# Performance work log

Hardware: AMD Instinct MI355X
Metric: run time of the kernel (lower is better)

## Reference

```python
import jax, jax.numpy as jnp
import numpy as np

N = 8192
F_IN = 256
F_OUT = 64
ALPHA = 0.2  # LeakyReLU negative slope
EDGE_P = 0.004  # ~33 avg degree


def setup_inputs() -> dict:
    key = jax.random.key(0)
    k1, k2, k3, k4 = jax.random.split(key, 4)
    h = jax.random.normal(k1, (N, F_IN), dtype=jnp.float32)
    # xavier-ish scale for params
    W = jax.random.normal(k2, (F_IN, F_OUT), dtype=jnp.float32) * np.float32(np.sqrt(2.0 / (F_IN + F_OUT)))
    a = jax.random.normal(k3, (2 * F_OUT, 1), dtype=jnp.float32) * np.float32(np.sqrt(2.0 / (2 * F_OUT + 1)))
    adj = (jax.random.uniform(k4, (N, N)) < EDGE_P).astype(jnp.float32)
    return {"h": h, "adj": adj, "W": W, "a": a}


def reference(h, adj, W, a):
    f_out = W.shape[1]
    Wh = h @ W  # [N, F_OUT]
    # NOTE: original uses a[out_features:] for the source (row) term
    wh1 = Wh @ a[f_out:, :]  # [N, 1]
    wh2 = Wh @ a[:f_out, :]  # [N, 1]
    # e[u, i] = wh1[u] + wh2[i] only where adj nonzero; zero elsewhere (NO -inf mask,
    # faithful to the original: softmax sees zeros at non-edges)
    e = jnp.where(adj != 0, wh1 + wh2.T, jnp.float32(0.0))  # [N, N]
    e = jnp.where(e >= 0, e, ALPHA * e)  # LeakyReLU
    attention = jax.nn.softmax(e, axis=1)  # [N, N]
    # dropout p=0.0 -> identity
    h_prime = attention @ Wh  # [N, F_OUT]
    return jax.nn.elu(h_prime)  # concat=True
```

## Files before the change

### kernel.cpp

```cpp
#include <hip/hip_runtime.h>
#include <hip/hip_bf16.h>
#include <math.h>

#define N     8192
#define F_IN  256
#define F_OUT 64
#define ALPHA 0.2f

__global__ __launch_bounds__(256) void gat_wh_kernel(
    const float* __restrict__ h,
    const float* __restrict__ W,
    const float* __restrict__ a,
    float* __restrict__ Wh,
    float* __restrict__ wh1,
    float* __restrict__ wh2,
    float* __restrict__ colpart)
{
    __shared__ float s_h[4][F_IN];
    __shared__ float s_cp[256];

    const int tid = threadIdx.x;
    const int wv  = tid >> 6;
    const int ln  = tid & 63;
    const int u   = blockIdx.x * 4 + wv;

    const float4* hrow = (const float4*)(h + (size_t)u * F_IN);
    ((float4*)s_h[wv])[ln] = hrow[ln];
    __syncthreads();

    float acc = 0.f;
    const float4* sh4 = (const float4*)s_h[wv];
#pragma unroll 8
    for (int k4 = 0; k4 < F_IN / 4; ++k4) {
        float4 hv = sh4[k4];
        int k = k4 * 4;
        acc += hv.x * W[(k + 0) * F_OUT + ln];
        acc += hv.y * W[(k + 1) * F_OUT + ln];
        acc += hv.z * W[(k + 2) * F_OUT + ln];
        acc += hv.w * W[(k + 3) * F_OUT + ln];
    }

    Wh[(size_t)u * F_OUT + ln] = acc;

    float p1 = acc * a[F_OUT + ln];
    float p2 = acc * a[ln];
#pragma unroll
    for (int off = 32; off > 0; off >>= 1) {
        p1 += __shfl_down(p1, off);
        p2 += __shfl_down(p2, off);
    }
    if (ln == 0) {
        wh1[u] = p1;
        wh2[u] = p2;
    }

    s_cp[tid] = acc;
    __syncthreads();
    if (tid < 64) {
        colpart[(size_t)blockIdx.x * 64 + tid] =
            s_cp[tid] + s_cp[tid + 64] + s_cp[tid + 128] + s_cp[tid + 192];
    }
}

__global__ __launch_bounds__(256) void gat_colsum_kernel(
    const float* __restrict__ colpart,
    float* __restrict__ colsum)
{
    __shared__ float r[256];
    const int f = blockIdx.x;
    const int tid = threadIdx.x;
    float s = 0.f;
    for (int b = tid; b < 2048; b += 256) s += colpart[(size_t)b * 64 + f];
    r[tid] = s;
    __syncthreads();
    if (tid < 128) r[tid] += r[tid + 128];
    __syncthreads();
    if (tid < 64) {
        float x = r[tid] + r[tid + 64];
#pragma unroll
        for (int off = 32; off > 0; off >>= 1) x += __shfl_down(x, off);
        if (tid == 0) colsum[f] = x;
    }
}

__global__ __launch_bounds__(256) void gat_main_kernel(
    const float* __restrict__ adj,
    const float* __restrict__ Wh,
    const float* __restrict__ wh1,
    const float* __restrict__ wh2,
    const float* __restrict__ colsum,
    float* __restrict__ out)
{
    const int tid  = threadIdx.x;
    const int lane = tid & 63;
    const int wv   = tid >> 6;
    const int u    = blockIdx.x * 4 + wv;

    const float wh1u = wh1[u];
    const float* __restrict__ arow = adj + (size_t)u * N;

    float acc  = 0.f;
    float sumw = 0.f;

    for (int it = 0; it < 16; ++it) {
        const int cbase = it * 512;
        const float4* p = (const float4*)(arow + cbase + lane * 8);
        float4 v0 = p[0];
        float4 v1 = p[1];
        float vals[8] = {v0.x, v0.y, v0.z, v0.w, v1.x, v1.y, v1.z, v1.w};
#pragma unroll
        for (int j = 0; j < 8; ++j) {
            unsigned long long m = __ballot(vals[j] != 0.f);
            while (m) {
                int l = __ffsll((long long)m) - 1;
                m &= m - 1;
                int col = cbase + l * 8 + j;
                float e = wh1u + wh2[col];
                e = (e >= 0.f) ? e : ALPHA * e;
                float w = expm1f(e);
                sumw += w;
                acc += w * Wh[(size_t)col * F_OUT + lane];
            }
        }
    }

    float val = (acc + colsum[lane]) / (sumw + (float)N);
    out[(size_t)u * F_OUT + lane] = (val > 0.f) ? val : expm1f(val);
}

extern "C" void kernel_launch(void* const* d_in, const int* in_sizes, int n_in,
                              void* d_out, int out_size, void* d_ws, size_t ws_size,
                              hipStream_t stream) {
    const float* h   = (const float*)d_in[0];
    const float* adj = (const float*)d_in[1];
    const float* W   = (const float*)d_in[2];
    const float* a   = (const float*)d_in[3];
    float* out = (float*)d_out;

    float* ws      = (float*)d_ws;
    float* Wh      = ws;
    float* wh1     = Wh + (size_t)N * F_OUT;
    float* wh2     = wh1 + N;
    float* colpart = wh2 + N;
    float* colsum  = colpart + 2048 * 64;

    gat_wh_kernel<<<N / 4, 256, 0, stream>>>(h, W, a, Wh, wh1, wh2, colpart);
    gat_colsum_kernel<<<64, 256, 0, stream>>>(colpart, colsum);
    gat_main_kernel<<<N / 4, 256, 0, stream>>>(adj, Wh, wh1, wh2, colsum, out);
}
```

Measured before the change: 395.2 us.

## Register-tile Wh GEMM over 8 rows, prefetch adjacency, compute edge weights in parallel

The projection kernel now handles 32 rows per block with 8 accumulators per thread, so each W load is reused across 8 rows and far fewer blocks are launched. The column-sum reduction shrinks to a single block. The main kernel widens each lane's adjacency chunk to 16 elements and prefetches the next chunk into registers. Each lane computes the attention weight for its own nonzero entry before the ballot loop and broadcasts it with a shuffle, which replaces the serialized exp computation per edge. This adds register pressure and extra shuffles in exchange for more load overlap and less serial work.

```diff
diff --git a/kernel.cpp b/kernel.cpp
--- a/kernel.cpp
+++ b/kernel.cpp
@@ -16,45 +16,55 @@
     float* __restrict__ wh2,
     float* __restrict__ colpart)
 {
-    __shared__ float s_h[4][F_IN];
+    __shared__ float s_h[32][F_IN];
     __shared__ float s_cp[256];
 
     const int tid = threadIdx.x;
     const int wv  = tid >> 6;
     const int ln  = tid & 63;
-    const int u   = blockIdx.x * 4 + wv;
+    const int rowbase = blockIdx.x * 32;
 
-    const float4* hrow = (const float4*)(h + (size_t)u * F_IN);
-    ((float4*)s_h[wv])[ln] = hrow[ln];
+    const float4* hsrc = (const float4*)(h + (size_t)rowbase * F_IN);
+    float4* hdst = (float4*)&s_h[0][0];
+#pragma unroll
+    for (int i = 0; i < 8; ++i) hdst[tid + 256 * i] = hsrc[tid + 256 * i];
     __syncthreads();
 
-    float acc = 0.f;
-    const float4* sh4 = (const float4*)s_h[wv];
-#pragma unroll 8
-    for (int k4 = 0; k4 < F_IN / 4; ++k4) {
-        float4 hv = sh4[k4];
-        int k = k4 * 4;
-        acc += hv.x * W[(k + 0) * F_OUT + ln];
-        acc += hv.y * W[(k + 1) * F_OUT + ln];
-        acc += hv.z * W[(k + 2) * F_OUT + ln];
-        acc += hv.w * W[(k + 3) * F_OUT + ln];
+    const int r0 = wv * 8;
+    float acc[8] = {0.f, 0.f, 0.f, 0.f, 0.f, 0.f, 0.f, 0.f};
+
+#pragma unroll 4
+    for (int k2 = 0; k2 < F_IN / 2; ++k2) {
+        const int k = k2 * 2;
+        const float wk0 = W[(k + 0) * F_OUT + ln];
+        const float wk1 = W[(k + 1) * F_OUT + ln];
+#pragma unroll
+        for (int r = 0; r < 8; ++r) {
+            const float2 hv = *(const float2*)&s_h[r0 + r][k];
+            acc[r] += hv.x * wk0 + hv.y * wk1;
+        }
     }
 
-    Wh[(size_t)u * F_OUT + ln] = acc;
+    const float a2 = a[ln];
+    const float a1 = a[F_OUT + ln];
+    float colacc = 0.f;
 
-    float p1 = acc * a[F_OUT + ln];
-    float p2 = acc * a[ln];
 #pragma unroll
-    for (int off = 32; off > 0; off >>= 1) {
-        p1 += __shfl_down(p1, off);
-        p2 += __shfl_down(p2, off);
-    }
-    if (ln == 0) {
-        wh1[u] = p1;
-        wh2[u] = p2;
+    for (int r = 0; r < 8; ++r) {
+        const int u = rowbase + r0 + r;
+        Wh[(size_t)u * F_OUT + ln] = acc[r];
+        colacc += acc[r];
+        float p1 = acc[r] * a1;
+        float p2 = acc[r] * a2;
+#pragma unroll
+        for (int off = 32; off > 0; off >>= 1) {
+            p1 += __shfl_down(p1, off);
+            p2 += __shfl_down(p2, off);
+        }
+        if (ln == 0) { wh1[u] = p1; wh2[u] = p2; }
     }
 
-    s_cp[tid] = acc;
+    s_cp[tid] = colacc;
     __syncthreads();
     if (tid < 64) {
         colpart[(size_t)blockIdx.x * 64 + tid] =
@@ -67,19 +77,15 @@
     float* __restrict__ colsum)
 {
     __shared__ float r[256];
-    const int f = blockIdx.x;
     const int tid = threadIdx.x;
+    const int f = tid & 63;
+    const int g = tid >> 6;
     float s = 0.f;
-    for (int b = tid; b < 2048; b += 256) s += colpart[(size_t)b * 64 + f];
+    for (int b = g; b < 256; b += 4) s += colpart[(size_t)b * 64 + f];
     r[tid] = s;
     __syncthreads();
-    if (tid < 128) r[tid] += r[tid + 128];
-    __syncthreads();
     if (tid < 64) {
-        float x = r[tid] + r[tid + 64];
-#pragma unroll
-        for (int off = 32; off > 0; off >>= 1) x += __shfl_down(x, off);
-        if (tid == 0) colsum[f] = x;
+        colsum[f] = r[f] + r[f + 64] + r[f + 128] + r[f + 192];
     }
 }
 
@@ -102,30 +108,41 @@
     float acc  = 0.f;
     float sumw = 0.f;
 
-    for (int it = 0; it < 16; ++it) {
-        const int cbase = it * 512;
-        const float4* p = (const float4*)(arow + cbase + lane * 8);
-        float4 v0 = p[0];
-        float4 v1 = p[1];
-        float vals[8] = {v0.x, v0.y, v0.z, v0.w, v1.x, v1.y, v1.z, v1.w};
+    const float4* p0 = (const float4*)arow + lane * 4;
+    float4 b0 = p0[0], b1 = p0[1], b2 = p0[2], b3 = p0[3];
+
+    for (int it = 0; it < 8; ++it) {
+        const float4 v0 = b0, v1 = b1, v2 = b2, v3 = b3;
+        if (it < 7) {
+            const float4* np = (const float4*)(arow + (it + 1) * 1024) + lane * 4;
+            b0 = np[0]; b1 = np[1]; b2 = np[2]; b3 = np[3];
+        }
+        const int cbase = it * 1024;
+        const float vals[16] = {v0.x, v0.y, v0.z, v0.w, v1.x, v1.y, v1.z, v1.w,
+                                v2.x, v2.y, v2.z, v2.w, v3.x, v3.y, v3.z, v3.w};
 #pragma unroll
-        for (int j = 0; j < 8; ++j) {
-            unsigned long long m = __ballot(vals[j] != 0.f);
+        for (int j = 0; j < 16; ++j) {
+            const bool nz = (vals[j] != 0.f);
+            float w_own = 0.f;
+            if (nz) {
+                float e = wh1u + wh2[cbase + lane * 16 + j];
+                e = (e >= 0.f) ? e : ALPHA * e;
+                w_own = expm1f(e);
+            }
+            unsigned long long m = __ballot(nz);
             while (m) {
-                int l = __ffsll((long long)m) - 1;
+                const int l = __ffsll((long long)m) - 1;
                 m &= m - 1;
-                int col = cbase + l * 8 + j;
-                float e = wh1u + wh2[col];
-                e = (e >= 0.f) ? e : ALPHA * e;
-                float w = expm1f(e);
+                const float w = __shfl(w_own, l);
+                const int col = cbase + (l << 4) + j;
                 sumw += w;
-                acc += w * Wh[(size_t)col * F_OUT + lane];
+                acc += w * Wh[((size_t)col << 6) + lane];
             }
         }
     }
 
-    float val = (acc + colsum[lane]) / (sumw + (float)N);
-    out[(size_t)u * F_OUT + lane] = (val > 0.f) ? val : expm1f(val);
+    const float val = (acc + colsum[lane]) / (sumw + (float)N);
+    out[((size_t)u << 6) + lane] = (val > 0.f) ? val : expm1f(val);
 }
 
 extern "C" void kernel_launch(void* const* d_in, const int* in_sizes, int n_in,
@@ -142,9 +159,9 @@
     float* wh1     = Wh + (size_t)N * F_OUT;
     float* wh2     = wh1 + N;
     float* colpart = wh2 + N;
-    float* colsum  = colpart + 2048 * 64;
+    float* colsum  = colpart + 256 * 64;
 
-    gat_wh_kernel<<<N / 4, 256, 0, stream>>>(h, W, a, Wh, wh1, wh2, colpart);
-    gat_colsum_kernel<<<64, 256, 0, stream>>>(colpart, colsum);
+    gat_wh_kernel<<<N / 32, 256, 0, stream>>>(h, W, a, Wh, wh1, wh2, colpart);
+    gat_colsum_kernel<<<1, 256, 0, stream>>>(colpart, colsum);
     gat_main_kernel<<<N / 4, 256, 0, stream>>>(adj, Wh, wh1, wh2, colsum, out);
 }
```

Result: slower. 415.8 us (+5.2%).

## Fuse GAT projection, column sum and attention into one cooperative kernel

Applied to the files above, without the earlier changes.

Merges the three kernels into a single cooperative launch of 1024 blocks, each handling 8 rows, with grid-wide syncs between the projection, column-sum and sparse attention phases. Each wave now computes two rows in the projection GEMV, so every W load is reused across both rows. The aim is to remove two kernel launch gaps and cut redundant W traffic. In exchange it adds two grid barriers, and the grid must be co-resident (1024 blocks at 4 per CU), which caps occupancy for the bandwidth-bound adjacency scan.

```diff
diff --git a/kernel.cpp b/kernel.cpp
--- a/kernel.cpp
+++ b/kernel.cpp
@@ -1,131 +1,142 @@
 #include <hip/hip_runtime.h>
+#include <hip/hip_cooperative_groups.h>
 #include <hip/hip_bf16.h>
 #include <math.h>
+
+namespace cg = cooperative_groups;
 
 #define N     8192
 #define F_IN  256
 #define F_OUT 64
 #define ALPHA 0.2f
+#define NBLK  1024
+#define RPB   8
 
-__global__ __launch_bounds__(256) void gat_wh_kernel(
+__global__ __launch_bounds__(256, 4) void gat_fused_kernel(
     const float* __restrict__ h,
+    const float* __restrict__ adj,
     const float* __restrict__ W,
     const float* __restrict__ a,
     float* __restrict__ Wh,
     float* __restrict__ wh1,
     float* __restrict__ wh2,
-    float* __restrict__ colpart)
+    float* __restrict__ colpart,
+    float* __restrict__ colsum,
+    float* __restrict__ out)
 {
-    __shared__ float s_h[4][F_IN];
+    __shared__ float s_h[RPB][F_IN];
     __shared__ float s_cp[256];
 
     const int tid = threadIdx.x;
     const int wv  = tid >> 6;
     const int ln  = tid & 63;
-    const int u   = blockIdx.x * 4 + wv;
+    const int rowbase = blockIdx.x * RPB;
 
-    const float4* hrow = (const float4*)(h + (size_t)u * F_IN);
-    ((float4*)s_h[wv])[ln] = hrow[ln];
+    {
+        const float4* hsrc = (const float4*)(h + (size_t)rowbase * F_IN);
+        float4* hdst = (float4*)&s_h[0][0];
+        hdst[tid]       = hsrc[tid];
+        hdst[tid + 256] = hsrc[tid + 256];
+    }
     __syncthreads();
 
-    float acc = 0.f;
-    const float4* sh4 = (const float4*)s_h[wv];
+    const int r0 = wv * 2;
+    float acc0 = 0.f, acc1 = 0.f;
 #pragma unroll 8
-    for (int k4 = 0; k4 < F_IN / 4; ++k4) {
-        float4 hv = sh4[k4];
-        int k = k4 * 4;
-        acc += hv.x * W[(k + 0) * F_OUT + ln];
-        acc += hv.y * W[(k + 1) * F_OUT + ln];
-        acc += hv.z * W[(k + 2) * F_OUT + ln];
-        acc += hv.w * W[(k + 3) * F_OUT + ln];
+    for (int k2 = 0; k2 < F_IN / 2; ++k2) {
+        const int k = k2 * 2;
+        const float wk0 = W[(k + 0) * F_OUT + ln];
+        const float wk1 = W[(k + 1) * F_OUT + ln];
+        const float2 h0 = *(const float2*)&s_h[r0 + 0][k];
+        const float2 h1 = *(const float2*)&s_h[r0 + 1][k];
+        acc0 += h0.x * wk0 + h0.y * wk1;
+        acc1 += h1.x * wk0 + h1.y * wk1;
     }
 
-    Wh[(size_t)u * F_OUT + ln] = acc;
-
-    float p1 = acc * a[F_OUT + ln];
-    float p2 = acc * a[ln];
+    {
+        const float a2 = a[ln];
+        const float a1 = a[F_OUT + ln];
+        const int u0 = rowbase + r0;
+        Wh[(size_t)u0 * F_OUT + ln]       = acc0;
+        Wh[(size_t)(u0 + 1) * F_OUT + ln] = acc1;
+        float p10 = acc0 * a1, p20 = acc0 * a2;
+        float p11 = acc1 * a1, p21 = acc1 * a2;
 #pragma unroll
-    for (int off = 32; off > 0; off >>= 1) {
-        p1 += __shfl_down(p1, off);
-        p2 += __shfl_down(p2, off);
-    }
-    if (ln == 0) {
-        wh1[u] = p1;
-        wh2[u] = p2;
+        for (int off = 32; off > 0; off >>= 1) {
+            p10 += __shfl_down(p10, off);
+            p20 += __shfl_down(p20, off);
+            p11 += __shfl_down(p11, off);
+            p21 += __shfl_down(p21, off);
+        }
+        if (ln == 0) {
+            wh1[u0] = p10;  wh2[u0] = p20;
+            wh1[u0 + 1] = p11;  wh2[u0 + 1] = p21;
+        }
     }
 
-    s_cp[tid] = acc;
+    s_cp[tid] = acc0 + acc1;
     __syncthreads();
     if (tid < 64) {
         colpart[(size_t)blockIdx.x * 64 + tid] =
             s_cp[tid] + s_cp[tid + 64] + s_cp[tid + 128] + s_cp[tid + 192];
     }
-}
 
-__global__ __launch_bounds__(256) void gat_colsum_kernel(
-    const float* __restrict__ colpart,
-    float* __restrict__ colsum)
-{
-    __shared__ float r[256];
-    const int f = blockIdx.x;
-    const int tid = threadIdx.x;
-    float s = 0.f;
-    for (int b = tid; b < 2048; b += 256) s += colpart[(size_t)b * 64 + f];
-    r[tid] = s;
-    __syncthreads();
-    if (tid < 128) r[tid] += r[tid + 128];
-    __syncthreads();
-    if (tid < 64) {
-        float x = r[tid] + r[tid + 64];
+    cg::this_grid().sync();
+
+    if (blockIdx.x < 64) {
+        const int f = blockIdx.x;
+        float s = 0.f;
+        for (int b = tid; b < NBLK; b += 256) s += colpart[(size_t)b * 64 + f];
+        s_cp[tid] = s;
+        __syncthreads();
+        if (tid < 128) s_cp[tid] += s_cp[tid + 128];
+        __syncthreads();
+        if (tid < 64) {
+            float x = s_cp[tid] + s_cp[tid + 64];
 #pragma unroll
-        for (int off = 32; off > 0; off >>= 1) x += __shfl_down(x, off);
-        if (tid == 0) colsum[f] = x;
-    }
-}
-
-__global__ __launch_bounds__(256) void gat_main_kernel(
-    const float* __restrict__ adj,
-    const float* __restrict__ Wh,
-    const float* __restrict__ wh1,
-    const float* __restrict__ wh2,
-    const float* __restrict__ colsum,
-    float* __restrict__ out)
-{
-    const int tid  = threadIdx.x;
-    const int lane = tid & 63;
-    const int wv   = tid >> 6;
-    const int u    = blockIdx.x * 4 + wv;
-
-    const float wh1u = wh1[u];
-    const float* __restrict__ arow = adj + (size_t)u * N;
-
-    float acc  = 0.f;
-    float sumw = 0.f;
-
-    for (int it = 0; it < 16; ++it) {
-        const int cbase = it * 512;
-        const float4* p = (const float4*)(arow + cbase + lane * 8);
-        float4 v0 = p[0];
-        float4 v1 = p[1];
-        float vals[8] = {v0.x, v0.y, v0.z, v0.w, v1.x, v1.y, v1.z, v1.w};
-#pragma unroll
-        for (int j = 0; j < 8; ++j) {
-            unsigned long long m = __ballot(vals[j] != 0.f);
-            while (m) {
-                int l = __ffsll((long long)m) - 1;
-                m &= m - 1;
-                int col = cbase + l * 8 + j;
-                float e = wh1u + wh2[col];
-                e = (e >= 0.f) ? e : ALPHA * e;
-                float w = expm1f(e);
-                sumw += w;
-                acc += w * Wh[(size_t)col * F_OUT + lane];
-            }
+            for (int off = 32; off > 0; off >>= 1) x += __shfl_down(x, off);
+            if (tid == 0) colsum[f] = x;
         }
     }
 
-    float val = (acc + colsum[lane]) / (sumw + (float)N);
-    out[(size_t)u * F_OUT + lane] = (val > 0.f) ? val : expm1f(val);
+    cg::this_grid().sync();
+
+    const float cs = colsum[ln];
+#pragma unroll
+    for (int r = 0; r < 2; ++r) {
+        const int u = rowbase + wv + 4 * r;
+        const float wh1u = wh1[u];
+        const float* __restrict__ arow = adj + (size_t)u * N;
+
+        float acc  = 0.f;
+        float sumw = 0.f;
+
+        for (int it = 0; it < 16; ++it) {
+            const int cbase = it * 512;
+            const float4* p = (const float4*)(arow + cbase + ln * 8);
+            const float4 v0 = p[0];
+            const float4 v1 = p[1];
+            const float vals[8] = {v0.x, v0.y, v0.z, v0.w,
+                                   v1.x, v1.y, v1.z, v1.w};
+#pragma unroll
+            for (int j = 0; j < 8; ++j) {
+                unsigned long long m = __ballot(vals[j] != 0.f);
+                while (m) {
+                    const int l = __ffsll((long long)m) - 1;
+                    m &= m - 1;
+                    const int col = cbase + l * 8 + j;
+                    float e = wh1u + wh2[col];
+                    e = (e >= 0.f) ? e : ALPHA * e;
+                    const float w = expm1f(e);
+                    sumw += w;
+                    acc += w * Wh[((size_t)col << 6) + ln];
+                }
+            }
+        }
+
+        const float val = (acc + cs) / (sumw + (float)N);
+        out[((size_t)u << 6) + ln] = (val > 0.f) ? val : expm1f(val);
+    }
 }
 
 extern "C" void kernel_launch(void* const* d_in, const int* in_sizes, int n_in,
@@ -142,9 +153,13 @@
     float* wh1     = Wh + (size_t)N * F_OUT;
     float* wh2     = wh1 + N;
     float* colpart = wh2 + N;
-    float* colsum  = colpart + 2048 * 64;
+    float* colsum  = colpart + (size_t)NBLK * 64;
 
-    gat_wh_kernel<<<N / 4, 256, 0, stream>>>(h, W, a, Wh, wh1, wh2, colpart);
-    gat_colsum_kernel<<<64, 256, 0, stream>>>(colpart, colsum);
-    gat_main_kernel<<<N / 4, 256, 0, stream>>>(adj, Wh, wh1, wh2, colsum, out);
+    void* args[] = {
+        (void*)&h, (void*)&adj, (void*)&W, (void*)&a,
+        (void*)&Wh, (void*)&wh1, (void*)&wh2,
+        (void*)&colpart, (void*)&colsum, (void*)&out
+    };
+    hipLaunchCooperativeKernel((const void*)gat_fused_kernel,
+                               dim3(NBLK), dim3(256), args, 0, stream);
 }
```

Result: slower. 555.6 us (+40.6%).
